# Kernel tuning notes

Hardware: AMD Instinct MI355X
Metric: run time of the kernel (lower is better)

Reference implementation:

```python
import jax, jax.numpy as jnp
import numpy as np

N = 50000   # nodes
E = 800000  # edges
F = 128     # num_features
H = 128     # embedding_size
C = 10      # num_classes
G = 64      # graphs in batch


def setup_inputs() -> dict:
    key = jax.random.key(0)
    ks = jax.random.split(key, 12)
    x = jax.random.normal(ks[0], (N, F), dtype=jnp.float32)
    edge_index = jax.random.randint(ks[1], (2, E), 0, N, dtype=jnp.int32)
    batch_index = jnp.sort(jax.random.randint(ks[2], (N,), 0, G, dtype=jnp.int32))

    def lin(k, fan_in, fan_out):
        s = 1.0 / np.sqrt(fan_in)
        kw, kb = jax.random.split(k)
        W = jax.random.uniform(kw, (fan_in, fan_out), jnp.float32, -s, s)
        b = jax.random.uniform(kb, (fan_out,), jnp.float32, -s, s)
        return W, b

    W0, b0 = lin(ks[3], F, H)
    W1, b1 = lin(ks[4], H, H)
    W2, b2 = lin(ks[5], H, H)
    Wa, ba = lin(ks[6], 2 * H, C)
    return {"x": x, "edge_index": edge_index, "batch_index": batch_index,
            "W0": W0, "b0": b0, "W1": W1, "b1": b1, "W2": W2, "b2": b2,
            "Wa": Wa, "ba": ba}


def gcn_conv(x, src, dst, inv_sqrt_deg, W, b):
    # PyG GCNConv: h = x @ W; out_i = sum_{j->i} h_j / sqrt(d_j d_i)
    # with added self loops (deg already includes +1; self-loop term = h_i / d_i).
    h = x @ W                                             # [N, H]
    coef = inv_sqrt_deg[src] * inv_sqrt_deg[dst]          # [E]
    msg = coef[:, None] * h[src]                          # [E, H]
    agg = jax.ops.segment_sum(msg, dst, num_segments=N)   # [N, H]
    agg = agg + (inv_sqrt_deg * inv_sqrt_deg)[:, None] * h  # self loops
    return agg + b


def reference(x, edge_index, batch_index, W0, b0, W1, b1, W2, b2, Wa, ba):
    src, dst = edge_index[0], edge_index[1]
    # degree including self loop
    deg = jax.ops.segment_sum(jnp.ones((E,), x.dtype), dst, num_segments=N) + 1.0
    inv_sqrt_deg = jax.lax.rsqrt(deg)

    h = jax.nn.relu(gcn_conv(x, src, dst, inv_sqrt_deg, W0, b0))
    h = jax.nn.relu(gcn_conv(h, src, dst, inv_sqrt_deg, W1, b1))
    h = jax.nn.relu(gcn_conv(h, src, dst, inv_sqrt_deg, W2, b2))

    counts = jax.ops.segment_sum(jnp.ones((N,), x.dtype), batch_index, num_segments=G)
    sums = jax.ops.segment_sum(h, batch_index, num_segments=G)
    mean = sums / jnp.maximum(counts, 1.0)[:, None]
    mx = jax.ops.segment_max(h, batch_index, num_segments=G)
    mx = jnp.where(counts[:, None] > 0, mx, 0.0)

    aggr = jnp.concatenate([mean, mx], axis=1)            # [G, 2H]
    out = aggr @ Wa + ba                                  # [G, C]
    return out, aggr
```

## Files before the change

kernel.cpp:

```cpp
#include <hip/hip_runtime.h>
#include <stdint.h>

#define N_NODES 50000
#define N_EDGES 800000
#define HID 128
#define NCLS 10
#define NGRAPH 64
#define CAP 64

typedef unsigned short ushort_t;
typedef __attribute__((ext_vector_type(8))) short bf16x8;
typedef __attribute__((ext_vector_type(4))) float f32x4;

__device__ __forceinline__ ushort_t f2bf(float f) {
    union { float f; unsigned int i; } v; v.f = f;
    unsigned int u = v.i;
    return (ushort_t)((u + 0x7FFFu + ((u >> 16) & 1u)) >> 16);
}
__device__ __forceinline__ float bf2f(ushort_t u) {
    union { unsigned int i; float f; } v; v.i = ((unsigned int)u) << 16; return v.f;
}
__device__ __forceinline__ void add4(float4& a, const float4& v) {
    a.x += v.x; a.y += v.y; a.z += v.z; a.w += v.w;
}
__device__ __forceinline__ void fmad4(float4& a, float d, const float4& v) {
    a.x = fmaf(d, v.x, a.x); a.y = fmaf(d, v.y, a.y);
    a.z = fmaf(d, v.z, a.z); a.w = fmaf(d, v.w, a.w);
}
__device__ __forceinline__ int exhi(int p) { return (p >> 16) & 0xffff; }
__device__ __forceinline__ int exlo(int p) { return p & 0xffff; }

__global__ void k_zero(int* cnt, float* sums, float* maxs,
                       const int* __restrict__ batch, int* bound, int* counts,
                       const float* __restrict__ W0, const float* __restrict__ W1,
                       const float* __restrict__ W2, ushort_t* Whi, ushort_t* Wlo) {
    int b = blockIdx.x, t = threadIdx.x;
    if (b < 196) {
        int i = b * 256 + t;
        if (i < N_NODES) cnt[i] = 0;
        if (i < NGRAPH * HID) { sums[i] = 0.f; maxs[i] = 0.f; }
    } else if (b == 196) {
        int g = t;
        if (g <= NGRAPH) {
            int lo = 0, hi = N_NODES;
            while (lo < hi) {
                int mid = (lo + hi) >> 1;
                if (batch[mid] < g) lo = mid + 1; else hi = mid;
            }
            bound[g] = lo;
        }
        __syncthreads();
        if (g < NGRAPH) counts[g] = bound[g + 1] - bound[g];
    } else {
        int gid = (b - 197) * 256 + t;
        int l = gid / (32 * 512);
        int rem = gid - l * 32 * 512;
        int tile = rem >> 9;
        int p = rem & 511;
        int lane = p >> 3, j = p & 7;
        int kk = tile >> 3, c = tile & 7;
        int k = 32 * kk + (lane >> 4) * 8 + j;
        int n = 16 * c + (lane & 15);
        const float* W = (l == 0) ? W0 : (l == 1) ? W1 : W2;
        float x = W[k * 128 + n];
        ushort_t hi = f2bf(x);
        ushort_t lo = f2bf(x - bf2f(hi));
        Whi[l * 16384 + rem] = hi;
        Wlo[l * 16384 + rem] = lo;
    }
}

__global__ void k_fill(const int* __restrict__ src, const int* __restrict__ dst,
                       int* cnt, ushort_t* csr16) {
    int base = (blockIdx.x * 256 + threadIdx.x) * 8;
    if (base + 7 < N_EDGES) {
        int4 da = *(const int4*)(dst + base);
        int4 db = *(const int4*)(dst + base + 4);
        int4 sa = *(const int4*)(src + base);
        int4 sb = *(const int4*)(src + base + 4);
        int p0 = atomicAdd(&cnt[da.x], 1);
        int p1 = atomicAdd(&cnt[da.y], 1);
        int p2 = atomicAdd(&cnt[da.z], 1);
        int p3 = atomicAdd(&cnt[da.w], 1);
        int p4 = atomicAdd(&cnt[db.x], 1);
        int p5 = atomicAdd(&cnt[db.y], 1);
        int p6 = atomicAdd(&cnt[db.z], 1);
        int p7 = atomicAdd(&cnt[db.w], 1);
        if (p0 < CAP) csr16[da.x * CAP + p0] = (ushort_t)sa.x;
        if (p1 < CAP) csr16[da.y * CAP + p1] = (ushort_t)sa.y;
        if (p2 < CAP) csr16[da.z * CAP + p2] = (ushort_t)sa.z;
        if (p3 < CAP) csr16[da.w * CAP + p3] = (ushort_t)sa.w;
        if (p4 < CAP) csr16[db.x * CAP + p4] = (ushort_t)sb.x;
        if (p5 < CAP) csr16[db.y * CAP + p5] = (ushort_t)sb.y;
        if (p6 < CAP) csr16[db.z * CAP + p6] = (ushort_t)sb.z;
        if (p7 < CAP) csr16[db.w * CAP + p7] = (ushort_t)sb.w;
    } else {
        for (int i = base; i < N_EDGES; i++) {
            int d = dst[i];
            int slot = atomicAdd(&cnt[d], 1);
            if (slot < CAP) csr16[d * CAP + slot] = (ushort_t)src[i];
        }
    }
}

__global__ void k_layer(const float* __restrict__ In, const ushort_t* __restrict__ csr16,
                        const int* __restrict__ cnt,
                        const ushort_t* __restrict__ Whi, const ushort_t* __restrict__ Wlo,
                        const float* __restrict__ bias, int pre_scaled, int scale_out,
                        int pool, const int* __restrict__ batch,
                        float* sums, float* maxs, float* __restrict__ Out) {
    __shared__ float T[16][132];
    __shared__ int sg[16];
    int t = threadIdx.x, wv = t >> 6, lane = t & 63;
    int hl = lane & 31, q = lane >> 5;
    if (pool && t < 16) sg[t] = batch[blockIdx.x * 16 + t];

    for (int r = 0; r < 4; r++) {
        int i = blockIdx.x * 16 + wv * 4 + r;
        int ci = cnt[i];
        int m = min(ci, CAP);
        float isdi = rsqrtf((float)ci + 1.0f);
        int packed = ((const int*)(csr16 + (size_t)i * CAP))[hl];
        float4 self = *(const float4*)(In + (size_t)i * 128 + hl * 4);
        float sfac = pre_scaled ? 1.0f : isdi;
        float4 a0 = make_float4(0.f, 0.f, 0.f, 0.f);
        float4 a1 = a0, a2 = a0, a3 = a0;
        if (q == 0) { a0.x = sfac * self.x; a0.y = sfac * self.y;
                      a0.z = sfac * self.z; a0.w = sfac * self.w; }
        int e = 0;
        if (pre_scaled) {
            for (; e + 7 < m; e += 8) {
                int k0 = e >> 1;
                int p0 = __shfl(packed, k0);
                int p1 = __shfl(packed, k0 + 1);
                int p2 = __shfl(packed, k0 + 2);
                int p3 = __shfl(packed, k0 + 3);
                int s0 = q ? exhi(p0) : exlo(p0);
                int s1 = q ? exhi(p1) : exlo(p1);
                int s2 = q ? exhi(p2) : exlo(p2);
                int s3 = q ? exhi(p3) : exlo(p3);
                float4 v0 = *(const float4*)(In + (size_t)s0 * 128 + hl * 4);
                float4 v1 = *(const float4*)(In + (size_t)s1 * 128 + hl * 4);
                float4 v2 = *(const float4*)(In + (size_t)s2 * 128 + hl * 4);
                float4 v3 = *(const float4*)(In + (size_t)s3 * 128 + hl * 4);
                add4(a0, v0); add4(a1, v1); add4(a2, v2); add4(a3, v3);
            }
            for (; e + 1 < m; e += 2) {
                int p = __shfl(packed, e >> 1);
                int s0 = q ? exhi(p) : exlo(p);
                float4 v0 = *(const float4*)(In + (size_t)s0 * 128 + hl * 4);
                add4(a0, v0);
            }
            if (e < m && q == 0) {
                int p = __shfl(packed, e >> 1);
                int s0 = exlo(p);
                float4 v0 = *(const float4*)(In + (size_t)s0 * 128 + hl * 4);
                add4(a0, v0);
            }
        } else {
            for (; e + 7 < m; e += 8) {
                int k0 = e >> 1;
                int p0 = __shfl(packed, k0);
                int p1 = __shfl(packed, k0 + 1);
                int p2 = __shfl(packed, k0 + 2);
                int p3 = __shfl(packed, k0 + 3);
                int s0 = q ? exhi(p0) : exlo(p0);
                int s1 = q ? exhi(p1) : exlo(p1);
                int s2 = q ? exhi(p2) : exlo(p2);
                int s3 = q ? exhi(p3) : exlo(p3);
                float d0 = rsqrtf((float)cnt[s0] + 1.0f);
                float d1 = rsqrtf((float)cnt[s1] + 1.0f);
                float d2 = rsqrtf((float)cnt[s2] + 1.0f);
                float d3 = rsqrtf((float)cnt[s3] + 1.0f);
                float4 v0 = *(const float4*)(In + (size_t)s0 * 128 + hl * 4);
                float4 v1 = *(const float4*)(In + (size_t)s1 * 128 + hl * 4);
                float4 v2 = *(const float4*)(In + (size_t)s2 * 128 + hl * 4);
                float4 v3 = *(const float4*)(In + (size_t)s3 * 128 + hl * 4);
                fmad4(a0, d0, v0); fmad4(a1, d1, v1);
                fmad4(a2, d2, v2); fmad4(a3, d3, v3);
            }
            for (; e + 1 < m; e += 2) {
                int p = __shfl(packed, e >> 1);
                int s0 = q ? exhi(p) : exlo(p);
                float d0 = rsqrtf((float)cnt[s0] + 1.0f);
                float4 v0 = *(const float4*)(In + (size_t)s0 * 128 + hl * 4);
                fmad4(a0, d0, v0);
            }
            if (e < m && q == 0) {
                int p = __shfl(packed, e >> 1);
                int s0 = exlo(p);
                float d0 = rsqrtf((float)cnt[s0] + 1.0f);
                float4 v0 = *(const float4*)(In + (size_t)s0 * 128 + hl * 4);
                fmad4(a0, d0, v0);
            }
        }
        float4 s4;
        s4.x = (a0.x + a1.x) + (a2.x + a3.x);
        s4.y = (a0.y + a1.y) + (a2.y + a3.y);
        s4.z = (a0.z + a1.z) + (a2.z + a3.z);
        s4.w = (a0.w + a1.w) + (a2.w + a3.w);
        s4.x += __shfl_xor(s4.x, 32);
        s4.y += __shfl_xor(s4.y, 32);
        s4.z += __shfl_xor(s4.z, 32);
        s4.w += __shfl_xor(s4.w, 32);
        if (q == 0) {
            float4 o;
            o.x = isdi * s4.x; o.y = isdi * s4.y;
            o.z = isdi * s4.z; o.w = isdi * s4.w;
            *(float4*)&T[wv * 4 + r][hl * 4] = o;
        }
    }
    __syncthreads();

    int mrow = lane & 15, qq = lane >> 4;
    f32x4 acc[2];
    acc[0] = (f32x4){0.f, 0.f, 0.f, 0.f};
    acc[1] = (f32x4){0.f, 0.f, 0.f, 0.f};
#pragma unroll
    for (int kk = 0; kk < 4; kk++) {
        const float* tp = &T[mrow][kk * 32 + qq * 8];
        float4 p0 = *(const float4*)tp;
        float4 p1 = *(const float4*)(tp + 4);
        float av[8] = {p0.x, p0.y, p0.z, p0.w, p1.x, p1.y, p1.z, p1.w};
        bf16x8 ahi, alo;
#pragma unroll
        for (int j = 0; j < 8; j++) {
            ushort_t hbits = f2bf(av[j]);
            ahi[j] = (short)hbits;
            alo[j] = (short)f2bf(av[j] - bf2f(hbits));
        }
#pragma unroll
        for (int cl = 0; cl < 2; cl++) {
            int c = wv * 2 + cl;
            const bf16x8 bhi = *(const bf16x8*)(Whi + (((kk * 8 + c) * 64 + lane) << 3));
            const bf16x8 blo = *(const bf16x8*)(Wlo + (((kk * 8 + c) * 64 + lane) << 3));
            acc[cl] = __builtin_amdgcn_mfma_f32_16x16x32_bf16(ahi, bhi, acc[cl], 0, 0, 0);
            acc[cl] = __builtin_amdgcn_mfma_f32_16x16x32_bf16(alo, bhi, acc[cl], 0, 0, 0);
            acc[cl] = __builtin_amdgcn_mfma_f32_16x16x32_bf16(ahi, blo, acc[cl], 0, 0, 0);
        }
    }
    int rb = blockIdx.x * 16 + qq * 4;
    if (!pool) {
        float osc[4];
#pragma unroll
        for (int rr = 0; rr < 4; rr++)
            osc[rr] = scale_out ? rsqrtf((float)cnt[rb + rr] + 1.0f) : 1.0f;
#pragma unroll
        for (int cl = 0; cl < 2; cl++) {
            int col = (wv * 2 + cl) * 16 + mrow;
            float bcol = bias[col];
#pragma unroll
            for (int rr = 0; rr < 4; rr++) {
                float val = fmaxf(acc[cl][rr] + bcol, 0.f);
                Out[(size_t)(rb + rr) * 128 + col] = val * osc[rr];
            }
        }
    } else {
        __syncthreads();
#pragma unroll
        for (int cl = 0; cl < 2; cl++) {
            int col = (wv * 2 + cl) * 16 + mrow;
            float bcol = bias[col];
#pragma unroll
            for (int rr = 0; rr < 4; rr++)
                T[qq * 4 + rr][col] = fmaxf(acc[cl][rr] + bcol, 0.f);
        }
        __syncthreads();
        int f = t & 127, half = t >> 7;
        int cur = sg[0];
        float s = 0.f, mx = 0.f;
        for (int r = 0; r < 16; r++) {
            int g = sg[r];
            if (g != cur) {
                if (half == 0) atomicAdd(&sums[cur * HID + f], s);
                else atomicMax((int*)&maxs[cur * HID + f], __float_as_int(mx));
                s = 0.f; mx = 0.f; cur = g;
            }
            float v = T[r][f];
            s += v;
            mx = fmaxf(mx, v);
        }
        if (half == 0) atomicAdd(&sums[cur * HID + f], s);
        else atomicMax((int*)&maxs[cur * HID + f], __float_as_int(mx));
    }
}

__global__ void k_final(const float* __restrict__ sums, const float* __restrict__ maxs,
                        const int* __restrict__ counts, const float* __restrict__ Wa,
                        const float* __restrict__ ba, float* __restrict__ out) {
    __shared__ float a[256];
    __shared__ float red[4];
    int g = blockIdx.x, t = threadIdx.x;
    float denom = fmaxf((float)counts[g], 1.f);
    float val = (t < 128) ? (sums[g * HID + t] / denom) : maxs[g * HID + (t - 128)];
    a[t] = val;
    out[NGRAPH * NCLS + g * 256 + t] = val;
    __syncthreads();
    for (int c = 0; c < NCLS; c++) {
        float p = a[t] * Wa[t * NCLS + c];
        for (int o = 32; o > 0; o >>= 1) p += __shfl_down(p, o);
        if ((t & 63) == 0) red[t >> 6] = p;
        __syncthreads();
        if (t == 0) {
            out[g * NCLS + c] = red[0] + red[1] + red[2] + red[3] + ba[c];
        }
        __syncthreads();
    }
}

extern "C" void kernel_launch(void* const* d_in, const int* in_sizes, int n_in,
                              void* d_out, int out_size, void* d_ws, size_t ws_size,
                              hipStream_t stream) {
    const float* x = (const float*)d_in[0];
    const int* ei = (const int*)d_in[1];
    const int* src = ei;
    const int* dst = ei + N_EDGES;
    const int* batch = (const int*)d_in[2];
    const float* W0 = (const float*)d_in[3];
    const float* b0 = (const float*)d_in[4];
    const float* W1 = (const float*)d_in[5];
    const float* b1 = (const float*)d_in[6];
    const float* W2 = (const float*)d_in[7];
    const float* b2 = (const float*)d_in[8];
    const float* Wa = (const float*)d_in[9];
    const float* ba = (const float*)d_in[10];
    float* out = (float*)d_out;

    char* ws = (char*)d_ws;
    int*      cnt    = (int*)(ws + 0);
    int*      bound  = (int*)(ws + 200192);
    int*      counts = (int*)(ws + 200576);
    float*    sums   = (float*)(ws + 200832);
    float*    maxs   = (float*)(ws + 233600);
    ushort_t* Whi    = (ushort_t*)(ws + 266368);
    ushort_t* Wlo    = (ushort_t*)(ws + 364672);
    ushort_t* csr16  = (ushort_t*)(ws + 462976);
    float*    h      = (float*)(ws + 6862976);
    float*    hp     = (float*)(ws + 32462976);

    k_zero<<<389, 256, 0, stream>>>(cnt, sums, maxs, batch, bound, counts,
                                    W0, W1, W2, Whi, Wlo);
    k_fill<<<391, 256, 0, stream>>>(src, dst, cnt, csr16);

    k_layer<<<3125, 256, 0, stream>>>(x, csr16, cnt, Whi, Wlo, b0, 0, 1,
                                      0, batch, sums, maxs, h);
    k_layer<<<3125, 256, 0, stream>>>(h, csr16, cnt, Whi + 16384, Wlo + 16384, b1, 1, 1,
                                      0, batch, sums, maxs, hp);
    k_layer<<<3125, 256, 0, stream>>>(hp, csr16, cnt, Whi + 32768, Wlo + 32768, b2, 1, 0,
                                      1, batch, sums, maxs, h);

    k_final<<<NGRAPH, 256, 0, stream>>>(sums, maxs, counts, Wa, ba, out);
}
```

Baseline: 321.6 us.

## Split GCN layers into feature-chunked aggregation and separate MFMA matmul kernels

Replaces the fused per-layer kernel with a pipeline: the input is relaid out into eight 16-feature column chunks pre-scaled by inverse sqrt degree. A dedicated gather-aggregate kernel then works one chunk at a time with atomic tile work-stealing, followed by a split-bf16 MFMA matmul kernel that writes chunked output. Aggregating before the matmul, with each chunk small enough to stay cache-resident, is meant to improve locality of the random neighbor gathers. In exchange it adds extra kernel launches, a larger workspace and extra full-tensor round trips through memory, and it falls back to the old path if the workspace is too small.

Result: slower. 467.8 us (+45.5%).

```diff
diff --git a/kernel.cpp b/kernel.cpp
--- a/kernel.cpp
+++ b/kernel.cpp
@@ -7,10 +7,17 @@
 #define NCLS 10
 #define NGRAPH 64
 #define CAP 64
+#define NCHUNK 8
+#define CHUNK_F 16
+#define CH_STRIDE (N_NODES * CHUNK_F)
+#define AGG_TILES 782
+#define AGG_GRID 1536
+#define NEW_WS_NEED 83662976
 
 typedef unsigned short ushort_t;
 typedef __attribute__((ext_vector_type(8))) short bf16x8;
 typedef __attribute__((ext_vector_type(4))) float f32x4;
+typedef __attribute__((ext_vector_type(4))) int i32x4;
 
 __device__ __forceinline__ ushort_t f2bf(float f) {
     union { float f; unsigned int i; } v; v.f = f;
@@ -33,7 +40,8 @@
 __global__ void k_zero(int* cnt, float* sums, float* maxs,
                        const int* __restrict__ batch, int* bound, int* counts,
                        const float* __restrict__ W0, const float* __restrict__ W1,
-                       const float* __restrict__ W2, ushort_t* Whi, ushort_t* Wlo) {
+                       const float* __restrict__ W2, ushort_t* Whi, ushort_t* Wlo,
+                       int* tctr) {
     int b = blockIdx.x, t = threadIdx.x;
     if (b < 196) {
         int i = b * 256 + t;
@@ -49,6 +57,7 @@
             }
             bound[g] = lo;
         }
+        if (t >= 128 && t < 152) tctr[t - 128] = 0;
         __syncthreads();
         if (g < NGRAPH) counts[g] = bound[g + 1] - bound[g];
     } else {
@@ -103,6 +112,189 @@
     }
 }
 
+__global__ void k_relayout(const float* __restrict__ x, const int* __restrict__ cnt,
+                           float* __restrict__ Xc) {
+    int gid = blockIdx.x * 256 + threadIdx.x;
+    int c = gid / 200000;
+    int r2 = gid - c * 200000;
+    int i = r2 >> 2, f4 = r2 & 3;
+    float isd = rsqrtf((float)cnt[i] + 1.0f);
+    f32x4 v = *(const f32x4*)(x + (size_t)i * HID + c * CHUNK_F + f4 * 4);
+    f32x4 o;
+    o.x = isd * v.x; o.y = isd * v.y; o.z = isd * v.z; o.w = isd * v.w;
+    __builtin_nontemporal_store(o, (f32x4*)(Xc + (size_t)c * CH_STRIDE + i * CHUNK_F + f4 * 4));
+}
+
+__global__ __launch_bounds__(256, 6)
+void k_agg(const float* __restrict__ Hc, const ushort_t* __restrict__ csr16,
+           const int* __restrict__ cnt, float* __restrict__ Agg, int* tctr) {
+    int c = blockIdx.x & 7;
+    int t = threadIdx.x;
+    int j = t & 3;
+    int bl = (t & 63) & ~3;
+    const float* chunk = Hc + (size_t)c * CH_STRIDE;
+    float* aggc = Agg + (size_t)c * CH_STRIDE;
+    __shared__ int stile;
+    for (;;) {
+        __syncthreads();
+        if (t == 0) stile = atomicAdd(tctr + c, 1);
+        __syncthreads();
+        int tile = stile;
+        if (tile >= AGG_TILES) break;
+        int i = tile * 64 + (t >> 2);
+        if (i < N_NODES) {
+            int ci = cnt[i];
+            int m = min(ci, CAP);
+            float isd = rsqrtf((float)ci + 1.0f);
+            const i32x4* row = (const i32x4*)(csr16 + (size_t)i * CAP);
+            i32x4 pk0 = __builtin_nontemporal_load(row + j);
+            i32x4 pk1;
+            if (m > 32) pk1 = __builtin_nontemporal_load(row + 4 + j);
+            f32x4 accA = *(const f32x4*)(chunk + i * CHUNK_F + j * 4);
+            f32x4 accB = (f32x4){0.f, 0.f, 0.f, 0.f};
+            int full = m >> 3, rem = m & 7;
+#pragma unroll
+            for (int o = 0; o < 8; ++o) {
+                if (o >= full) break;
+                i32x4 pks = (o < 4) ? pk0 : pk1;
+                int sl = bl + (o & 3);
+                int px = __shfl(pks.x, sl), py = __shfl(pks.y, sl);
+                int pz = __shfl(pks.z, sl), pw = __shfl(pks.w, sl);
+                int s0 = exlo(px), s1 = exhi(px);
+                int s2 = exlo(py), s3 = exhi(py);
+                int s4 = exlo(pz), s5 = exhi(pz);
+                int s6 = exlo(pw), s7 = exhi(pw);
+                f32x4 v0 = *(const f32x4*)(chunk + s0 * CHUNK_F + j * 4);
+                f32x4 v1 = *(const f32x4*)(chunk + s1 * CHUNK_F + j * 4);
+                f32x4 v2 = *(const f32x4*)(chunk + s2 * CHUNK_F + j * 4);
+                f32x4 v3 = *(const f32x4*)(chunk + s3 * CHUNK_F + j * 4);
+                f32x4 v4 = *(const f32x4*)(chunk + s4 * CHUNK_F + j * 4);
+                f32x4 v5 = *(const f32x4*)(chunk + s5 * CHUNK_F + j * 4);
+                f32x4 v6 = *(const f32x4*)(chunk + s6 * CHUNK_F + j * 4);
+                f32x4 v7 = *(const f32x4*)(chunk + s7 * CHUNK_F + j * 4);
+                accA += (v0 + v1) + (v2 + v3);
+                accB += (v4 + v5) + (v6 + v7);
+            }
+            if (rem) {
+                int o = full;
+                i32x4 pks = (o < 4) ? pk0 : pk1;
+                int sl = bl + (o & 3);
+                int px = __shfl(pks.x, sl), py = __shfl(pks.y, sl);
+                int pz = __shfl(pks.z, sl), pw = __shfl(pks.w, sl);
+#pragma unroll
+                for (int k = 0; k < 7; ++k) {
+                    if (k < rem) {
+                        int comp = k >> 1;
+                        int pv = comp == 0 ? px : comp == 1 ? py : comp == 2 ? pz : pw;
+                        int s = (k & 1) ? exhi(pv) : exlo(pv);
+                        accB += *(const f32x4*)(chunk + s * CHUNK_F + j * 4);
+                    }
+                }
+            }
+            f32x4 o4;
+            o4.x = isd * (accA.x + accB.x);
+            o4.y = isd * (accA.y + accB.y);
+            o4.z = isd * (accA.z + accB.z);
+            o4.w = isd * (accA.w + accB.w);
+            __builtin_nontemporal_store(o4, (f32x4*)(aggc + i * CHUNK_F + j * 4));
+        }
+    }
+}
+
+__global__ void k_mm(const float* __restrict__ A, const int* __restrict__ cnt,
+                     const ushort_t* __restrict__ Whi, const ushort_t* __restrict__ Wlo,
+                     const float* __restrict__ bias, int scale_out, int pool,
+                     const int* __restrict__ batch, float* sums, float* maxs,
+                     float* __restrict__ Out) {
+    __shared__ float T[16][132];
+    __shared__ int sg[16];
+    int t = threadIdx.x, wv = t >> 6, lane = t & 63;
+    if (pool && t < 16) sg[t] = batch[blockIdx.x * 16 + t];
+#pragma unroll
+    for (int u = 0; u < 2; ++u) {
+        int idx = u * 256 + t;
+        int cch = idx >> 6, nn = (idx >> 2) & 15, f4q = idx & 3;
+        int node = blockIdx.x * 16 + nn;
+        f32x4 v = __builtin_nontemporal_load(
+            (const f32x4*)(A + (size_t)cch * CH_STRIDE + node * CHUNK_F + f4q * 4));
+        *(f32x4*)&T[nn][cch * 16 + f4q * 4] = v;
+    }
+    __syncthreads();
+
+    int mrow = lane & 15, qq = lane >> 4;
+    f32x4 acc[2];
+    acc[0] = (f32x4){0.f, 0.f, 0.f, 0.f};
+    acc[1] = (f32x4){0.f, 0.f, 0.f, 0.f};
+#pragma unroll
+    for (int kk = 0; kk < 4; kk++) {
+        const float* tp = &T[mrow][kk * 32 + qq * 8];
+        float4 p0 = *(const float4*)tp;
+        float4 p1 = *(const float4*)(tp + 4);
+        float av[8] = {p0.x, p0.y, p0.z, p0.w, p1.x, p1.y, p1.z, p1.w};
+        bf16x8 ahi, alo;
+#pragma unroll
+        for (int jj = 0; jj < 8; jj++) {
+            ushort_t hbits = f2bf(av[jj]);
+            ahi[jj] = (short)hbits;
+            alo[jj] = (short)f2bf(av[jj] - bf2f(hbits));
+        }
+#pragma unroll
+        for (int cl = 0; cl < 2; cl++) {
+            int c = wv * 2 + cl;
+            const bf16x8 bhi = *(const bf16x8*)(Whi + (((kk * 8 + c) * 64 + lane) << 3));
+            const bf16x8 blo = *(const bf16x8*)(Wlo + (((kk * 8 + c) * 64 + lane) << 3));
+            acc[cl] = __builtin_amdgcn_mfma_f32_16x16x32_bf16(ahi, bhi, acc[cl], 0, 0, 0);
+            acc[cl] = __builtin_amdgcn_mfma_f32_16x16x32_bf16(alo, bhi, acc[cl], 0, 0, 0);
+            acc[cl] = __builtin_amdgcn_mfma_f32_16x16x32_bf16(ahi, blo, acc[cl], 0, 0, 0);
+        }
+    }
+    int rb = blockIdx.x * 16 + qq * 4;
+    if (!pool) {
+        float osc[4];
+#pragma unroll
+        for (int rr = 0; rr < 4; rr++)
+            osc[rr] = scale_out ? rsqrtf((float)cnt[rb + rr] + 1.0f) : 1.0f;
+#pragma unroll
+        for (int cl = 0; cl < 2; cl++) {
+            int cc = wv * 2 + cl;
+            float bcol = bias[cc * 16 + mrow];
+#pragma unroll
+            for (int rr = 0; rr < 4; rr++) {
+                float val = fmaxf(acc[cl][rr] + bcol, 0.f) * osc[rr];
+                __builtin_nontemporal_store(val,
+                    Out + (size_t)cc * CH_STRIDE + (size_t)(rb + rr) * CHUNK_F + mrow);
+            }
+        }
+    } else {
+        __syncthreads();
+#pragma unroll
+        for (int cl = 0; cl < 2; cl++) {
+            int col = (wv * 2 + cl) * 16 + mrow;
+            float bcol = bias[col];
+#pragma unroll
+            for (int rr = 0; rr < 4; rr++)
+                T[qq * 4 + rr][col] = fmaxf(acc[cl][rr] + bcol, 0.f);
+        }
+        __syncthreads();
+        int f = t & 127, half = t >> 7;
+        int cur = sg[0];
+        float s = 0.f, mx = 0.f;
+        for (int r = 0; r < 16; r++) {
+            int g = sg[r];
+            if (g != cur) {
+                if (half == 0) atomicAdd(&sums[cur * HID + f], s);
+                else atomicMax((int*)&maxs[cur * HID + f], __float_as_int(mx));
+                s = 0.f; mx = 0.f; cur = g;
+            }
+            float v = T[r][f];
+            s += v;
+            mx = fmaxf(mx, v);
+        }
+        if (half == 0) atomicAdd(&sums[cur * HID + f], s);
+        else atomicMax((int*)&maxs[cur * HID + f], __float_as_int(mx));
+    }
+}
+
 __global__ void k_layer(const float* __restrict__ In, const ushort_t* __restrict__ csr16,
                         const int* __restrict__ cnt,
                         const ushort_t* __restrict__ Whi, const ushort_t* __restrict__ Wlo,
@@ -329,25 +521,40 @@
     char* ws = (char*)d_ws;
     int*      cnt    = (int*)(ws + 0);
     int*      bound  = (int*)(ws + 200192);
+    int*      tctr   = (int*)(ws + 200464);
     int*      counts = (int*)(ws + 200576);
     float*    sums   = (float*)(ws + 200832);
     float*    maxs   = (float*)(ws + 233600);
     ushort_t* Whi    = (ushort_t*)(ws + 266368);
     ushort_t* Wlo    = (ushort_t*)(ws + 364672);
     ushort_t* csr16  = (ushort_t*)(ws + 462976);
-    float*    h      = (float*)(ws + 6862976);
-    float*    hp     = (float*)(ws + 32462976);
+    float*    bufX   = (float*)(ws + 6862976);
+    float*    bufA   = (float*)(ws + 32462976);
+    float*    bufB   = (float*)(ws + 58062976);
 
     k_zero<<<389, 256, 0, stream>>>(cnt, sums, maxs, batch, bound, counts,
-                                    W0, W1, W2, Whi, Wlo);
+                                    W0, W1, W2, Whi, Wlo, tctr);
     k_fill<<<391, 256, 0, stream>>>(src, dst, cnt, csr16);
 
-    k_layer<<<3125, 256, 0, stream>>>(x, csr16, cnt, Whi, Wlo, b0, 0, 1,
-                                      0, batch, sums, maxs, h);
-    k_layer<<<3125, 256, 0, stream>>>(h, csr16, cnt, Whi + 16384, Wlo + 16384, b1, 1, 1,
-                                      0, batch, sums, maxs, hp);
-    k_layer<<<3125, 256, 0, stream>>>(hp, csr16, cnt, Whi + 32768, Wlo + 32768, b2, 1, 0,
-                                      1, batch, sums, maxs, h);
+    if (ws_size >= (size_t)NEW_WS_NEED) {
+        k_relayout<<<6250, 256, 0, stream>>>(x, cnt, bufX);
+        k_agg<<<AGG_GRID, 256, 0, stream>>>(bufX, csr16, cnt, bufA, tctr);
+        k_mm<<<3125, 256, 0, stream>>>(bufA, cnt, Whi, Wlo, b0, 1, 0,
+                                       batch, sums, maxs, bufB);
+        k_agg<<<AGG_GRID, 256, 0, stream>>>(bufB, csr16, cnt, bufA, tctr + 8);
+        k_mm<<<3125, 256, 0, stream>>>(bufA, cnt, Whi + 16384, Wlo + 16384, b1, 1, 0,
+                                       batch, sums, maxs, bufX);
+        k_agg<<<AGG_GRID, 256, 0, stream>>>(bufX, csr16, cnt, bufA, tctr + 16);
+        k_mm<<<3125, 256, 0, stream>>>(bufA, cnt, Whi + 32768, Wlo + 32768, b2, 0, 1,
+                                       batch, sums, maxs, bufB);
+    } else {
+        k_layer<<<3125, 256, 0, stream>>>(x, csr16, cnt, Whi, Wlo, b0, 0, 1,
+                                          0, batch, sums, maxs, bufX);
+        k_layer<<<3125, 256, 0, stream>>>(bufX, csr16, cnt, Whi + 16384, Wlo + 16384, b1, 1, 1,
+                                          0, batch, sums, maxs, bufA);
+        k_layer<<<3125, 256, 0, stream>>>(bufA, csr16, cnt, Whi + 32768, Wlo + 32768, b2, 1, 0,
+                                          1, batch, sums, maxs, bufX);
+    }
 
     k_final<<<NGRAPH, 256, 0, stream>>>(sums, maxs, counts, Wa, ba, out);
 }
```

## Store node features as per-row int16 with scale to halve gather traffic

Applied to the files above, without the earlier changes.

Adds a conversion kernel that quantizes the degree-prescaled input features to int16 with one float scale per row. Each layer now emits its activations in the same int16-plus-scale format, with the normalization folded into the scale. The gather loop reads 8-byte short4 vectors and dequantizes them with an FMA, so the bandwidth-bound neighbor gathers move half the bytes of fp32. The cost is an extra kernel launch and pass over x, an LDS staging round trip in each layer's epilogue, and some quantization error.

Result: faster. 283.9 us (-11.7%).

```diff
diff --git a/kernel.cpp b/kernel.cpp
--- a/kernel.cpp
+++ b/kernel.cpp
@@ -10,6 +10,8 @@
 
 typedef unsigned short ushort_t;
 typedef __attribute__((ext_vector_type(8))) short bf16x8;
+typedef __attribute__((ext_vector_type(8))) short s16x8;
+typedef __attribute__((ext_vector_type(4))) short s16x4;
 typedef __attribute__((ext_vector_type(4))) float f32x4;
 
 __device__ __forceinline__ ushort_t f2bf(float f) {
@@ -20,15 +22,14 @@
 __device__ __forceinline__ float bf2f(ushort_t u) {
     union { unsigned int i; float f; } v; v.i = ((unsigned int)u) << 16; return v.f;
 }
-__device__ __forceinline__ void add4(float4& a, const float4& v) {
-    a.x += v.x; a.y += v.y; a.z += v.z; a.w += v.w;
-}
-__device__ __forceinline__ void fmad4(float4& a, float d, const float4& v) {
-    a.x = fmaf(d, v.x, a.x); a.y = fmaf(d, v.y, a.y);
-    a.z = fmaf(d, v.z, a.z); a.w = fmaf(d, v.w, a.w);
-}
 __device__ __forceinline__ int exhi(int p) { return (p >> 16) & 0xffff; }
 __device__ __forceinline__ int exlo(int p) { return p & 0xffff; }
+__device__ __forceinline__ void fmad4q(float4& a, float c, s16x4 v) {
+    a.x = fmaf(c, (float)v[0], a.x);
+    a.y = fmaf(c, (float)v[1], a.y);
+    a.z = fmaf(c, (float)v[2], a.z);
+    a.w = fmaf(c, (float)v[3], a.w);
+}
 
 __global__ void k_zero(int* cnt, float* sums, float* maxs,
                        const int* __restrict__ batch, int* bound, int* counts,
@@ -103,12 +104,31 @@
     }
 }
 
-__global__ void k_layer(const float* __restrict__ In, const ushort_t* __restrict__ csr16,
-                        const int* __restrict__ cnt,
+__global__ void k_cvt(const float* __restrict__ x, const int* __restrict__ cnt,
+                      short* __restrict__ X16, float* __restrict__ Rs) {
+    int w = (blockIdx.x * 256 + threadIdx.x) >> 6;
+    int l = threadIdx.x & 63;
+    float isd = rsqrtf((float)cnt[w] + 1.0f);
+    float2 v = *(const float2*)(x + (size_t)w * HID + l * 2);
+    float a = isd * v.x, b = isd * v.y;
+    float m = fmaxf(fabsf(a), fabsf(b));
+#pragma unroll
+    for (int o = 1; o < 64; o <<= 1) m = fmaxf(m, __shfl_xor(m, o));
+    float sdec = fmaxf(m, 1e-20f) * (1.0f / 32767.0f);
+    float inv = 1.0f / sdec;
+    int q0 = (int)rintf(a * inv);
+    int q1 = (int)rintf(b * inv);
+    ((int*)(X16 + (size_t)w * HID))[l] = (q0 & 0xffff) | (q1 << 16);
+    if (l == 0) Rs[w] = sdec;
+}
+
+__global__ void k_layer(const short* __restrict__ In, const float* __restrict__ Rs,
+                        const ushort_t* __restrict__ csr16, const int* __restrict__ cnt,
                         const ushort_t* __restrict__ Whi, const ushort_t* __restrict__ Wlo,
-                        const float* __restrict__ bias, int pre_scaled, int scale_out,
+                        const float* __restrict__ bias, int scale_out,
                         int pool, const int* __restrict__ batch,
-                        float* sums, float* maxs, float* __restrict__ Out) {
+                        float* sums, float* maxs,
+                        short* __restrict__ Out, float* __restrict__ RsOut) {
     __shared__ float T[16][132];
     __shared__ int sg[16];
     int t = threadIdx.x, wv = t >> 6, lane = t & 63;
@@ -121,78 +141,48 @@
         int m = min(ci, CAP);
         float isdi = rsqrtf((float)ci + 1.0f);
         int packed = ((const int*)(csr16 + (size_t)i * CAP))[hl];
-        float4 self = *(const float4*)(In + (size_t)i * 128 + hl * 4);
-        float sfac = pre_scaled ? 1.0f : isdi;
         float4 a0 = make_float4(0.f, 0.f, 0.f, 0.f);
         float4 a1 = a0, a2 = a0, a3 = a0;
-        if (q == 0) { a0.x = sfac * self.x; a0.y = sfac * self.y;
-                      a0.z = sfac * self.z; a0.w = sfac * self.w; }
+        if (q == 0) {
+            float cs = Rs[i];
+            s16x4 sv = *(const s16x4*)(In + (size_t)i * HID + hl * 4);
+            fmad4q(a0, cs, sv);
+        }
         int e = 0;
-        if (pre_scaled) {
-            for (; e + 7 < m; e += 8) {
-                int k0 = e >> 1;
-                int p0 = __shfl(packed, k0);
-                int p1 = __shfl(packed, k0 + 1);
-                int p2 = __shfl(packed, k0 + 2);
-                int p3 = __shfl(packed, k0 + 3);
-                int s0 = q ? exhi(p0) : exlo(p0);
-                int s1 = q ? exhi(p1) : exlo(p1);
-                int s2 = q ? exhi(p2) : exlo(p2);
-                int s3 = q ? exhi(p3) : exlo(p3);
-                float4 v0 = *(const float4*)(In + (size_t)s0 * 128 + hl * 4);
-                float4 v1 = *(const float4*)(In + (size_t)s1 * 128 + hl * 4);
-                float4 v2 = *(const float4*)(In + (size_t)s2 * 128 + hl * 4);
-                float4 v3 = *(const float4*)(In + (size_t)s3 * 128 + hl * 4);
-                add4(a0, v0); add4(a1, v1); add4(a2, v2); add4(a3, v3);
-            }
-            for (; e + 1 < m; e += 2) {
-                int p = __shfl(packed, e >> 1);
-                int s0 = q ? exhi(p) : exlo(p);
-                float4 v0 = *(const float4*)(In + (size_t)s0 * 128 + hl * 4);
-                add4(a0, v0);
-            }
-            if (e < m && q == 0) {
-                int p = __shfl(packed, e >> 1);
-                int s0 = exlo(p);
-                float4 v0 = *(const float4*)(In + (size_t)s0 * 128 + hl * 4);
-                add4(a0, v0);
-            }
-        } else {
-            for (; e + 7 < m; e += 8) {
-                int k0 = e >> 1;
-                int p0 = __shfl(packed, k0);
-                int p1 = __shfl(packed, k0 + 1);
-                int p2 = __shfl(packed, k0 + 2);
-                int p3 = __shfl(packed, k0 + 3);
-                int s0 = q ? exhi(p0) : exlo(p0);
-                int s1 = q ? exhi(p1) : exlo(p1);
-                int s2 = q ? exhi(p2) : exlo(p2);
-                int s3 = q ? exhi(p3) : exlo(p3);
-                float d0 = rsqrtf((float)cnt[s0] + 1.0f);
-                float d1 = rsqrtf((float)cnt[s1] + 1.0f);
-                float d2 = rsqrtf((float)cnt[s2] + 1.0f);
-                float d3 = rsqrtf((float)cnt[s3] + 1.0f);
-                float4 v0 = *(const float4*)(In + (size_t)s0 * 128 + hl * 4);
-                float4 v1 = *(const float4*)(In + (size_t)s1 * 128 + hl * 4);
-                float4 v2 = *(const float4*)(In + (size_t)s2 * 128 + hl * 4);
-                float4 v3 = *(const float4*)(In + (size_t)s3 * 128 + hl * 4);
-                fmad4(a0, d0, v0); fmad4(a1, d1, v1);
-                fmad4(a2, d2, v2); fmad4(a3, d3, v3);
-            }
-            for (; e + 1 < m; e += 2) {
-                int p = __shfl(packed, e >> 1);
-                int s0 = q ? exhi(p) : exlo(p);
-                float d0 = rsqrtf((float)cnt[s0] + 1.0f);
-                float4 v0 = *(const float4*)(In + (size_t)s0 * 128 + hl * 4);
-                fmad4(a0, d0, v0);
-            }
-            if (e < m && q == 0) {
-                int p = __shfl(packed, e >> 1);
-                int s0 = exlo(p);
-                float d0 = rsqrtf((float)cnt[s0] + 1.0f);
-                float4 v0 = *(const float4*)(In + (size_t)s0 * 128 + hl * 4);
-                fmad4(a0, d0, v0);
-            }
+        for (; e + 7 < m; e += 8) {
+            int k0 = e >> 1;
+            int p0 = __shfl(packed, k0);
+            int p1 = __shfl(packed, k0 + 1);
+            int p2 = __shfl(packed, k0 + 2);
+            int p3 = __shfl(packed, k0 + 3);
+            int s0 = q ? exhi(p0) : exlo(p0);
+            int s1 = q ? exhi(p1) : exlo(p1);
+            int s2 = q ? exhi(p2) : exlo(p2);
+            int s3 = q ? exhi(p3) : exlo(p3);
+            float c0 = Rs[s0];
+            float c1 = Rs[s1];
+            float c2 = Rs[s2];
+            float c3 = Rs[s3];
+            s16x4 v0 = *(const s16x4*)(In + (size_t)s0 * HID + hl * 4);
+            s16x4 v1 = *(const s16x4*)(In + (size_t)s1 * HID + hl * 4);
+            s16x4 v2 = *(const s16x4*)(In + (size_t)s2 * HID + hl * 4);
+            s16x4 v3 = *(const s16x4*)(In + (size_t)s3 * HID + hl * 4);
+            fmad4q(a0, c0, v0); fmad4q(a1, c1, v1);
+            fmad4q(a2, c2, v2); fmad4q(a3, c3, v3);
+        }
+        for (; e + 1 < m; e += 2) {
+            int p = __shfl(packed, e >> 1);
+            int s0 = q ? exhi(p) : exlo(p);
+            float c0 = Rs[s0];
+            s16x4 v0 = *(const s16x4*)(In + (size_t)s0 * HID + hl * 4);
+            fmad4q(a0, c0, v0);
+        }
+        if (e < m && q == 0) {
+            int p = __shfl(packed, e >> 1);
+            int s0 = exlo(p);
+            float c0 = Rs[s0];
+            s16x4 v0 = *(const s16x4*)(In + (size_t)s0 * HID + hl * 4);
+            fmad4q(a0, c0, v0);
         }
         float4 s4;
         s4.x = (a0.x + a1.x) + (a2.x + a3.x);
@@ -245,16 +235,38 @@
 #pragma unroll
         for (int rr = 0; rr < 4; rr++)
             osc[rr] = scale_out ? rsqrtf((float)cnt[rb + rr] + 1.0f) : 1.0f;
+        __syncthreads();
 #pragma unroll
         for (int cl = 0; cl < 2; cl++) {
             int col = (wv * 2 + cl) * 16 + mrow;
             float bcol = bias[col];
 #pragma unroll
-            for (int rr = 0; rr < 4; rr++) {
-                float val = fmaxf(acc[cl][rr] + bcol, 0.f);
-                Out[(size_t)(rb + rr) * 128 + col] = val * osc[rr];
-            }
-        }
+            for (int rr = 0; rr < 4; rr++)
+                T[qq * 4 + rr][col] = fmaxf(acc[cl][rr] + bcol, 0.f) * osc[rr];
+        }
+        __syncthreads();
+        int rr2 = t >> 4, ll = t & 15;
+        const float* tp = &T[rr2][ll * 8];
+        float4 v0 = *(const float4*)tp;
+        float4 v1 = *(const float4*)(tp + 4);
+        float mxv = fmaxf(fmaxf(fmaxf(v0.x, v0.y), fmaxf(v0.z, v0.w)),
+                          fmaxf(fmaxf(v1.x, v1.y), fmaxf(v1.z, v1.w)));
+#pragma unroll
+        for (int o = 1; o < 16; o <<= 1) mxv = fmaxf(mxv, __shfl_xor(mxv, o));
+        float sdec = fmaxf(mxv, 1e-20f) * (1.0f / 32767.0f);
+        float inv = 1.0f / sdec;
+        s16x8 qv;
+        qv[0] = (short)(int)rintf(v0.x * inv);
+        qv[1] = (short)(int)rintf(v0.y * inv);
+        qv[2] = (short)(int)rintf(v0.z * inv);
+        qv[3] = (short)(int)rintf(v0.w * inv);
+        qv[4] = (short)(int)rintf(v1.x * inv);
+        qv[5] = (short)(int)rintf(v1.y * inv);
+        qv[6] = (short)(int)rintf(v1.z * inv);
+        qv[7] = (short)(int)rintf(v1.w * inv);
+        int orow = blockIdx.x * 16 + rr2;
+        *(s16x8*)(Out + (size_t)orow * HID + ll * 8) = qv;
+        if (ll == 0) RsOut[orow] = sdec;
     } else {
         __syncthreads();
 #pragma unroll
@@ -335,19 +347,24 @@
     ushort_t* Whi    = (ushort_t*)(ws + 266368);
     ushort_t* Wlo    = (ushort_t*)(ws + 364672);
     ushort_t* csr16  = (ushort_t*)(ws + 462976);
-    float*    h      = (float*)(ws + 6862976);
-    float*    hp     = (float*)(ws + 32462976);
+    float*    RsX    = (float*)(ws + 6862976);
+    float*    RsA    = (float*)(ws + 7062976);
+    float*    RsB    = (float*)(ws + 7262976);
+    short*    X16    = (short*)(ws + 7462976);
+    short*    hA     = (short*)(ws + 20262976);
+    short*    hB     = (short*)(ws + 33062976);
 
     k_zero<<<389, 256, 0, stream>>>(cnt, sums, maxs, batch, bound, counts,
                                     W0, W1, W2, Whi, Wlo);
     k_fill<<<391, 256, 0, stream>>>(src, dst, cnt, csr16);
-
-    k_layer<<<3125, 256, 0, stream>>>(x, csr16, cnt, Whi, Wlo, b0, 0, 1,
-                                      0, batch, sums, maxs, h);
-    k_layer<<<3125, 256, 0, stream>>>(h, csr16, cnt, Whi + 16384, Wlo + 16384, b1, 1, 1,
-                                      0, batch, sums, maxs, hp);
-    k_layer<<<3125, 256, 0, stream>>>(hp, csr16, cnt, Whi + 32768, Wlo + 32768, b2, 1, 0,
-                                      1, batch, sums, maxs, h);
+    k_cvt<<<12500, 256, 0, stream>>>(x, cnt, X16, RsX);
+
+    k_layer<<<3125, 256, 0, stream>>>(X16, RsX, csr16, cnt, Whi, Wlo, b0, 1,
+                                      0, batch, sums, maxs, hA, RsA);
+    k_layer<<<3125, 256, 0, stream>>>(hA, RsA, csr16, cnt, Whi + 16384, Wlo + 16384, b1, 1,
+                                      0, batch, sums, maxs, hB, RsB);
+    k_layer<<<3125, 256, 0, stream>>>(hB, RsB, csr16, cnt, Whi + 32768, Wlo + 32768, b2, 0,
+                                      1, batch, sums, maxs, hA, RsA);
 
     k_final<<<NGRAPH, 256, 0, stream>>>(sums, maxs, counts, Wa, ba, out);
 }
```

## Store node features in fp16 and pre-scale input to halve gather traffic

Applied to the files above, without the earlier changes.

Adds a conversion kernel that scales x by the inverse sqrt degree and stores it as fp16. Layer outputs are also written in fp16, and the gather loop reads f16x4 while accumulating in fp32. This roughly halves the bytes moved by the memory-bound neighbour gathers and drops the per-neighbour degree lookups from the first layer. It costs an extra kernel pass over x and adds fp16 rounding error to the activations.

New measurement: 271.9 us. -15.5%, faster.

```diff
diff --git a/kernel.cpp b/kernel.cpp
--- a/kernel.cpp
+++ b/kernel.cpp
@@ -11,6 +11,8 @@
 typedef unsigned short ushort_t;
 typedef __attribute__((ext_vector_type(8))) short bf16x8;
 typedef __attribute__((ext_vector_type(4))) float f32x4;
+typedef __attribute__((ext_vector_type(4))) _Float16 f16x4;
+typedef __attribute__((ext_vector_type(8))) _Float16 f16x8;
 
 __device__ __forceinline__ ushort_t f2bf(float f) {
     union { float f; unsigned int i; } v; v.f = f;
@@ -20,15 +22,14 @@
 __device__ __forceinline__ float bf2f(ushort_t u) {
     union { unsigned int i; float f; } v; v.i = ((unsigned int)u) << 16; return v.f;
 }
-__device__ __forceinline__ void add4(float4& a, const float4& v) {
-    a.x += v.x; a.y += v.y; a.z += v.z; a.w += v.w;
-}
-__device__ __forceinline__ void fmad4(float4& a, float d, const float4& v) {
-    a.x = fmaf(d, v.x, a.x); a.y = fmaf(d, v.y, a.y);
-    a.z = fmaf(d, v.z, a.z); a.w = fmaf(d, v.w, a.w);
-}
 __device__ __forceinline__ int exhi(int p) { return (p >> 16) & 0xffff; }
 __device__ __forceinline__ int exlo(int p) { return p & 0xffff; }
+__device__ __forceinline__ void add4h(float4& a, f16x4 v) {
+    a.x += (float)v[0];
+    a.y += (float)v[1];
+    a.z += (float)v[2];
+    a.w += (float)v[3];
+}
 
 __global__ void k_zero(int* cnt, float* sums, float* maxs,
                        const int* __restrict__ batch, int* bound, int* counts,
@@ -103,12 +104,27 @@
     }
 }
 
-__global__ void k_layer(const float* __restrict__ In, const ushort_t* __restrict__ csr16,
-                        const int* __restrict__ cnt,
+__global__ void k_cvt(const float* __restrict__ x, const int* __restrict__ cnt,
+                      _Float16* __restrict__ X16) {
+    int gid = blockIdx.x * 256 + threadIdx.x;
+    int i = gid >> 4, seg = gid & 15;
+    float isd = rsqrtf((float)cnt[i] + 1.0f);
+    const f32x4* px = (const f32x4*)(x + (size_t)i * HID + seg * 8);
+    f32x4 a = px[0], b = px[1];
+    f16x8 o;
+    o[0] = (_Float16)(isd * a.x); o[1] = (_Float16)(isd * a.y);
+    o[2] = (_Float16)(isd * a.z); o[3] = (_Float16)(isd * a.w);
+    o[4] = (_Float16)(isd * b.x); o[5] = (_Float16)(isd * b.y);
+    o[6] = (_Float16)(isd * b.z); o[7] = (_Float16)(isd * b.w);
+    *(f16x8*)(X16 + (size_t)i * HID + seg * 8) = o;
+}
+
+__global__ void k_layer(const _Float16* __restrict__ In,
+                        const ushort_t* __restrict__ csr16, const int* __restrict__ cnt,
                         const ushort_t* __restrict__ Whi, const ushort_t* __restrict__ Wlo,
-                        const float* __restrict__ bias, int pre_scaled, int scale_out,
+                        const float* __restrict__ bias, int scale_out,
                         int pool, const int* __restrict__ batch,
-                        float* sums, float* maxs, float* __restrict__ Out) {
+                        float* sums, float* maxs, _Float16* __restrict__ Out) {
     __shared__ float T[16][132];
     __shared__ int sg[16];
     int t = threadIdx.x, wv = t >> 6, lane = t & 63;
@@ -121,78 +137,40 @@
         int m = min(ci, CAP);
         float isdi = rsqrtf((float)ci + 1.0f);
         int packed = ((const int*)(csr16 + (size_t)i * CAP))[hl];
-        float4 self = *(const float4*)(In + (size_t)i * 128 + hl * 4);
-        float sfac = pre_scaled ? 1.0f : isdi;
         float4 a0 = make_float4(0.f, 0.f, 0.f, 0.f);
         float4 a1 = a0, a2 = a0, a3 = a0;
-        if (q == 0) { a0.x = sfac * self.x; a0.y = sfac * self.y;
-                      a0.z = sfac * self.z; a0.w = sfac * self.w; }
+        if (q == 0) {
+            f16x4 sv = *(const f16x4*)(In + (size_t)i * HID + hl * 4);
+            add4h(a0, sv);
+        }
         int e = 0;
-        if (pre_scaled) {
-            for (; e + 7 < m; e += 8) {
-                int k0 = e >> 1;
-                int p0 = __shfl(packed, k0);
-                int p1 = __shfl(packed, k0 + 1);
-                int p2 = __shfl(packed, k0 + 2);
-                int p3 = __shfl(packed, k0 + 3);
-                int s0 = q ? exhi(p0) : exlo(p0);
-                int s1 = q ? exhi(p1) : exlo(p1);
-                int s2 = q ? exhi(p2) : exlo(p2);
-                int s3 = q ? exhi(p3) : exlo(p3);
-                float4 v0 = *(const float4*)(In + (size_t)s0 * 128 + hl * 4);
-                float4 v1 = *(const float4*)(In + (size_t)s1 * 128 + hl * 4);
-                float4 v2 = *(const float4*)(In + (size_t)s2 * 128 + hl * 4);
-                float4 v3 = *(const float4*)(In + (size_t)s3 * 128 + hl * 4);
-                add4(a0, v0); add4(a1, v1); add4(a2, v2); add4(a3, v3);
-            }
-            for (; e + 1 < m; e += 2) {
-                int p = __shfl(packed, e >> 1);
-                int s0 = q ? exhi(p) : exlo(p);
-                float4 v0 = *(const float4*)(In + (size_t)s0 * 128 + hl * 4);
-                add4(a0, v0);
-            }
-            if (e < m && q == 0) {
-                int p = __shfl(packed, e >> 1);
-                int s0 = exlo(p);
-                float4 v0 = *(const float4*)(In + (size_t)s0 * 128 + hl * 4);
-                add4(a0, v0);
-            }
-        } else {
-            for (; e + 7 < m; e += 8) {
-                int k0 = e >> 1;
-                int p0 = __shfl(packed, k0);
-                int p1 = __shfl(packed, k0 + 1);
-                int p2 = __shfl(packed, k0 + 2);
-                int p3 = __shfl(packed, k0 + 3);
-                int s0 = q ? exhi(p0) : exlo(p0);
-                int s1 = q ? exhi(p1) : exlo(p1);
-                int s2 = q ? exhi(p2) : exlo(p2);
-                int s3 = q ? exhi(p3) : exlo(p3);
-                float d0 = rsqrtf((float)cnt[s0] + 1.0f);
-                float d1 = rsqrtf((float)cnt[s1] + 1.0f);
-                float d2 = rsqrtf((float)cnt[s2] + 1.0f);
-                float d3 = rsqrtf((float)cnt[s3] + 1.0f);
-                float4 v0 = *(const float4*)(In + (size_t)s0 * 128 + hl * 4);
-                float4 v1 = *(const float4*)(In + (size_t)s1 * 128 + hl * 4);
-                float4 v2 = *(const float4*)(In + (size_t)s2 * 128 + hl * 4);
-                float4 v3 = *(const float4*)(In + (size_t)s3 * 128 + hl * 4);
-                fmad4(a0, d0, v0); fmad4(a1, d1, v1);
-                fmad4(a2, d2, v2); fmad4(a3, d3, v3);
-            }
-            for (; e + 1 < m; e += 2) {
-                int p = __shfl(packed, e >> 1);
-                int s0 = q ? exhi(p) : exlo(p);
-                float d0 = rsqrtf((float)cnt[s0] + 1.0f);
-                float4 v0 = *(const float4*)(In + (size_t)s0 * 128 + hl * 4);
-                fmad4(a0, d0, v0);
-            }
-            if (e < m && q == 0) {
-                int p = __shfl(packed, e >> 1);
-                int s0 = exlo(p);
-                float d0 = rsqrtf((float)cnt[s0] + 1.0f);
-                float4 v0 = *(const float4*)(In + (size_t)s0 * 128 + hl * 4);
-                fmad4(a0, d0, v0);
-            }
+        for (; e + 7 < m; e += 8) {
+            int k0 = e >> 1;
+            int p0 = __shfl(packed, k0);
+            int p1 = __shfl(packed, k0 + 1);
+            int p2 = __shfl(packed, k0 + 2);
+            int p3 = __shfl(packed, k0 + 3);
+            int s0 = q ? exhi(p0) : exlo(p0);
+            int s1 = q ? exhi(p1) : exlo(p1);
+            int s2 = q ? exhi(p2) : exlo(p2);
+            int s3 = q ? exhi(p3) : exlo(p3);
+            f16x4 v0 = *(const f16x4*)(In + (size_t)s0 * HID + hl * 4);
+            f16x4 v1 = *(const f16x4*)(In + (size_t)s1 * HID + hl * 4);
+            f16x4 v2 = *(const f16x4*)(In + (size_t)s2 * HID + hl * 4);
+            f16x4 v3 = *(const f16x4*)(In + (size_t)s3 * HID + hl * 4);
+            add4h(a0, v0); add4h(a1, v1); add4h(a2, v2); add4h(a3, v3);
+        }
+        for (; e + 1 < m; e += 2) {
+            int p = __shfl(packed, e >> 1);
+            int s0 = q ? exhi(p) : exlo(p);
+            f16x4 v0 = *(const f16x4*)(In + (size_t)s0 * HID + hl * 4);
+            add4h(a0, v0);
+        }
+        if (e < m && q == 0) {
+            int p = __shfl(packed, e >> 1);
+            int s0 = exlo(p);
+            f16x4 v0 = *(const f16x4*)(In + (size_t)s0 * HID + hl * 4);
+            add4h(a0, v0);
         }
         float4 s4;
         s4.x = (a0.x + a1.x) + (a2.x + a3.x);
@@ -252,7 +230,7 @@
 #pragma unroll
             for (int rr = 0; rr < 4; rr++) {
                 float val = fmaxf(acc[cl][rr] + bcol, 0.f);
-                Out[(size_t)(rb + rr) * 128 + col] = val * osc[rr];
+                Out[(size_t)(rb + rr) * HID + col] = (_Float16)(val * osc[rr]);
             }
         }
     } else {
@@ -327,27 +305,29 @@
     float* out = (float*)d_out;
 
     char* ws = (char*)d_ws;
-    int*      cnt    = (int*)(ws + 0);
-    int*      bound  = (int*)(ws + 200192);
-    int*      counts = (int*)(ws + 200576);
-    float*    sums   = (float*)(ws + 200832);
-    float*    maxs   = (float*)(ws + 233600);
-    ushort_t* Whi    = (ushort_t*)(ws + 266368);
-    ushort_t* Wlo    = (ushort_t*)(ws + 364672);
-    ushort_t* csr16  = (ushort_t*)(ws + 462976);
-    float*    h      = (float*)(ws + 6862976);
-    float*    hp     = (float*)(ws + 32462976);
+    int*       cnt    = (int*)(ws + 0);
+    int*       bound  = (int*)(ws + 200192);
+    int*       counts = (int*)(ws + 200576);
+    float*     sums   = (float*)(ws + 200832);
+    float*     maxs   = (float*)(ws + 233600);
+    ushort_t*  Whi    = (ushort_t*)(ws + 266368);
+    ushort_t*  Wlo    = (ushort_t*)(ws + 364672);
+    ushort_t*  csr16  = (ushort_t*)(ws + 462976);
+    _Float16*  X16    = (_Float16*)(ws + 7462976);
+    _Float16*  hA     = (_Float16*)(ws + 20262976);
+    _Float16*  hB     = (_Float16*)(ws + 33062976);
 
     k_zero<<<389, 256, 0, stream>>>(cnt, sums, maxs, batch, bound, counts,
                                     W0, W1, W2, Whi, Wlo);
     k_fill<<<391, 256, 0, stream>>>(src, dst, cnt, csr16);
-
-    k_layer<<<3125, 256, 0, stream>>>(x, csr16, cnt, Whi, Wlo, b0, 0, 1,
-                                      0, batch, sums, maxs, h);
-    k_layer<<<3125, 256, 0, stream>>>(h, csr16, cnt, Whi + 16384, Wlo + 16384, b1, 1, 1,
-                                      0, batch, sums, maxs, hp);
-    k_layer<<<3125, 256, 0, stream>>>(hp, csr16, cnt, Whi + 32768, Wlo + 32768, b2, 1, 0,
-                                      1, batch, sums, maxs, h);
+    k_cvt<<<3125, 256, 0, stream>>>(x, cnt, X16);
+
+    k_layer<<<3125, 256, 0, stream>>>(X16, csr16, cnt, Whi, Wlo, b0, 1,
+                                      0, batch, sums, maxs, hA);
+    k_layer<<<3125, 256, 0, stream>>>(hA, csr16, cnt, Whi + 16384, Wlo + 16384, b1, 1,
+                                      0, batch, sums, maxs, hB);
+    k_layer<<<3125, 256, 0, stream>>>(hB, csr16, cnt, Whi + 32768, Wlo + 32768, b2, 0,
+                                      1, batch, sums, maxs, hA);
 
     k_final<<<NGRAPH, 256, 0, stream>>>(sums, maxs, counts, Wa, ba, out);
 }
```
